# Performance work log

Hardware: AMD Instinct MI355X
Metric: run time of the kernel (lower is better)

Reference implementation:

```python
import jax, jax.numpy as jnp
import numpy as np

TOKENS, IN_F, OUT_F = 8192, 4096, 16384


def setup_inputs() -> dict:
    key = jax.random.key(0)
    k1, k2, k3, k4 = jax.random.split(key, 4)
    input = jax.random.normal(k1, (TOKENS, IN_F), dtype=jnp.float32)
    # int8 quantized weight, stored [out_features, in_features] like the torch buffer
    weight = jax.random.randint(k2, (OUT_F, IN_F), -127, 128, dtype=jnp.int8)
    # per-output-channel dequant scale
    weight_scale = jax.random.uniform(k3, (OUT_F,), dtype=jnp.float32, minval=0.001, maxval=0.02)
    bias = jax.random.normal(k4, (OUT_F,), dtype=jnp.float32) * 0.01
    return {"input": input, "weight": weight, "weight_scale": weight_scale, "bias": bias}


def reference(input, weight, weight_scale, bias):
    # Fallback path of DynamicQuantizeMatMul: dequantize B = weight.T * scale, then matmul.
    # B: [in_features, out_features]; scale broadcasts over out_features (columns).
    B = weight.astype(jnp.float32).T * weight_scale
    out = input @ B + bias  # [tokens, out_features]
    return out
```

## Files before the change

kernel.cpp:

```cpp
#include <hip/hip_runtime.h>

#define MDIM 8192
#define NDIM 16384
#define KDIM 4096

typedef int i32x4 __attribute__((ext_vector_type(4)));
typedef int i32x16 __attribute__((ext_vector_type(16)));
typedef float f32x4 __attribute__((ext_vector_type(4)));

__device__ __forceinline__ unsigned short f2bf(float f) {
  __bf16 h = (__bf16)f;
  return __builtin_bit_cast(unsigned short, h);
}

__device__ __forceinline__ void gload_lds16(const void* g, void* l) {
  __builtin_amdgcn_global_load_lds(
      (const __attribute__((address_space(1))) unsigned int*)g,
      (__attribute__((address_space(3))) unsigned int*)l, 16, 0, 0);
}


__global__ __launch_bounds__(256) void cvt_a_q8(const float* __restrict__ a,
                                                signed char* __restrict__ o,
                                                float* __restrict__ sA) {
  const int row = blockIdx.x;
  const int tid = threadIdx.x;
  float v[16];
  const float4* s4 = (const float4*)(a + (long long)row * KDIM + tid * 16);
#pragma unroll
  for (int i = 0; i < 4; ++i) {
    float4 f = s4[i];
    v[i * 4 + 0] = f.x; v[i * 4 + 1] = f.y;
    v[i * 4 + 2] = f.z; v[i * 4 + 3] = f.w;
  }
  float m = 0.f;
#pragma unroll
  for (int i = 0; i < 16; ++i) m = fmaxf(m, fabsf(v[i]));
#pragma unroll
  for (int off = 32; off; off >>= 1) m = fmaxf(m, __shfl_xor(m, off));
  __shared__ float red[4];
  if ((tid & 63) == 0) red[tid >> 6] = m;
  __syncthreads();
  m = fmaxf(fmaxf(red[0], red[1]), fmaxf(red[2], red[3]));
  const float inv = m > 0.f ? 127.f / m : 0.f;
  if (tid == 0) sA[row] = m * (1.f / 127.f);
  union { signed char c[16]; uint4 u; } p;
#pragma unroll
  for (int i = 0; i < 16; ++i)
    p.c[i] = (signed char)__float2int_rn(v[i] * inv);
  const int kt = tid >> 2, ks = tid & 3;
  *(uint4*)(o + ((((long long)(row >> 8) * 64 + kt) * 4 + ks) << 12) +
            ((row & 255) << 4)) = p.u;
}

__global__ __launch_bounds__(256) void cvt_w_q8(const int* __restrict__ w,
                                                signed char* __restrict__ o) {
  const int nt = blockIdx.x >> 6;
  const int kt = blockIdx.x & 63;
  const int t = threadIdx.x;
  const int* src = w + (long long)(nt * 256 + t) * KDIM + kt * 64;
  signed char* dst = o + (((long long)(nt * 64 + kt) * 4) << 12) + (t << 4);
#pragma unroll
  for (int ks = 0; ks < 4; ++ks) {
    union { signed char c[16]; uint4 u; } p;
#pragma unroll
    for (int i = 0; i < 4; ++i) {
      int4 x = *(const int4*)(src + ks * 16 + i * 4);
      p.c[i * 4 + 0] = (signed char)x.x; p.c[i * 4 + 1] = (signed char)x.y;
      p.c[i * 4 + 2] = (signed char)x.z; p.c[i * 4 + 3] = (signed char)x.w;
    }
    *(uint4*)(dst + (ks << 12)) = p.u;
  }
}

__global__ __launch_bounds__(512, 2) void gemm_i8_v13(
    const signed char* __restrict__ Ab, const signed char* __restrict__ Wb,
    const float* __restrict__ sA, const float* __restrict__ sc,
    const float* __restrict__ bi, float* __restrict__ out) {
  __shared__ alignas(16) char sm[3 * 32768];
  const int tid = threadIdx.x;
  const int lane = tid & 63;
  const int wv = tid >> 6;
  const int l31 = lane & 31;
  const int l32 = lane >> 5;
  const int wr = wv >> 2;
  const int wc = wv & 3;
  const int c = blockIdx.x & 7;
  const int l = blockIdx.x >> 3;
  const int mA = ((c & 3) << 3) + (l & 7);
  const int nT = ((c >> 2) << 5) + (l >> 3);
  const int bm = mA << 8;
  const int bn = nT << 8;

  int aO[2][4], bO[2][2];
#pragma unroll
  for (int kk = 0; kk < 2; ++kk) {
#pragma unroll
    for (int mb = 0; mb < 4; ++mb)
      aO[kk][mb] = (kk * 2 + l32) * 4096 + (wr * 128 + mb * 32 + l31) * 16;
#pragma unroll
    for (int nb = 0; nb < 2; ++nb)
      bO[kk][nb] = 16384 + (kk * 2 + l32) * 4096 + (wc * 64 + nb * 32 + l31) * 16;
  }

  i32x16 acc[4][2] = {};

  const signed char* aSrc = Ab + ((long long)mA << 20) + (tid << 4);
  const signed char* bSrc = Wb + ((long long)nT << 20) + (tid << 4);
  const int t16 = tid << 4;

  char* bR = &sm[0];
  char* bN = &sm[32768];
  char* bS = &sm[65536];

  auto STAGE = [&](char* slot) {
    gload_lds16(aSrc, slot + t16);
    gload_lds16(aSrc + 8192, slot + 8192 + t16);
    gload_lds16(bSrc, slot + 16384 + t16);
    gload_lds16(bSrc + 8192, slot + 24576 + t16);
    aSrc += 16384;
    bSrc += 16384;
  };

  STAGE(bR);
  STAGE(bN);
  asm volatile("s_waitcnt vmcnt(4)" ::: "memory");
  __builtin_amdgcn_s_barrier();

  for (int t = 0; t < 64; ++t) {
    if (t <= 61) STAGE(bS);
    __builtin_amdgcn_s_setprio(1);
    i32x4 aF[2][4], bF[2][2];
#pragma unroll
    for (int kk = 0; kk < 2; ++kk) {
#pragma unroll
      for (int mb = 0; mb < 4; ++mb) aF[kk][mb] = *(const i32x4*)(bR + aO[kk][mb]);
#pragma unroll
      for (int nb = 0; nb < 2; ++nb) bF[kk][nb] = *(const i32x4*)(bR + bO[kk][nb]);
    }
#pragma unroll
    for (int kk = 0; kk < 2; ++kk)
#pragma unroll
      for (int mb = 0; mb < 4; ++mb)
#pragma unroll
        for (int nb = 0; nb < 2; ++nb)
          acc[mb][nb] = __builtin_amdgcn_mfma_i32_32x32x32_i8(
              aF[kk][mb], bF[kk][nb], acc[mb][nb], 0, 0, 0);
    __builtin_amdgcn_s_setprio(0);
    if (t <= 61) {
      asm volatile("s_waitcnt vmcnt(4)" ::: "memory");
    } else if (t == 62) {
      asm volatile("s_waitcnt vmcnt(0)" ::: "memory");
    }
    if (t < 63) __builtin_amdgcn_s_barrier();
    char* tmp = bR; bR = bN; bN = bS; bS = tmp;
  }

  float sv[2], bv[2];
#pragma unroll
  for (int nb = 0; nb < 2; ++nb) {
    const int cc = bn + wc * 64 + nb * 32 + l31;
    sv[nb] = sc[cc];
    bv[nb] = bi[cc];
  }
#pragma unroll
  for (int mb = 0; mb < 4; ++mb) {
    const int rb = bm + wr * 128 + mb * 32 + l32 * 4;
    float sa[16];
#pragma unroll
    for (int r = 0; r < 16; ++r) sa[r] = sA[rb + (r & 3) + 8 * (r >> 2)];
#pragma unroll
    for (int nb = 0; nb < 2; ++nb) {
      const int cc = bn + wc * 64 + nb * 32 + l31;
#pragma unroll
      for (int r = 0; r < 16; ++r) {
        const long long row = rb + (r & 3) + 8 * (r >> 2);
        __builtin_nontemporal_store(
            (float)acc[mb][nb][r] * (sa[r] * sv[nb]) + bv[nb],
            out + row * NDIM + cc);
      }
    }
  }
}

__global__ __launch_bounds__(256, 2) void gemm_inline(
    const float* __restrict__ A, const int* __restrict__ W,
    const float* __restrict__ sc, const float* __restrict__ bi,
    float* __restrict__ out) {
  typedef __bf16 bf16x8 __attribute__((ext_vector_type(8)));
  __shared__ unsigned short As[128 * 72];
  __shared__ unsigned short Bs[128 * 72];
  const int tid = threadIdx.x;
  const int lane = tid & 63;
  const int wv = tid >> 6;
  const int wg = (blockIdx.x & 7) * 1024 + (blockIdx.x >> 3);
  const int bm = (wg & 63) * 128;
  const int bn = (wg >> 6) * 128;
  const int wr = (wv >> 1) * 64;
  const int wc = (wv & 1) * 64;
  const int r16 = lane & 15;
  const int g4 = lane >> 4;

  f32x4 acc[4][4] = {};

  const int srow = tid >> 4;
  const int sc4 = (tid & 15) << 2;
  const float* aPtr = A + (long long)(bm + srow) * KDIM + sc4;
  const int* wPtr = W + (long long)(bn + srow) * KDIM + sc4;

  for (int kt = 0; kt < KDIM; kt += 64) {
    float4 av[8];
    int4 wv4[8];
#pragma unroll
    for (int j = 0; j < 8; ++j)
      av[j] = *(const float4*)(aPtr + (long long)j * 16 * KDIM + kt);
#pragma unroll
    for (int j = 0; j < 8; ++j)
      wv4[j] = *(const int4*)(wPtr + (long long)j * 16 * KDIM + kt);
    __syncthreads();
#pragma unroll
    for (int j = 0; j < 8; ++j) {
      ushort4 u;
      u.x = f2bf(av[j].x); u.y = f2bf(av[j].y);
      u.z = f2bf(av[j].z); u.w = f2bf(av[j].w);
      *(ushort4*)&As[(srow + j * 16) * 72 + sc4] = u;
    }
#pragma unroll
    for (int j = 0; j < 8; ++j) {
      ushort4 u;
      u.x = f2bf((float)wv4[j].x); u.y = f2bf((float)wv4[j].y);
      u.z = f2bf((float)wv4[j].z); u.w = f2bf((float)wv4[j].w);
      *(ushort4*)&Bs[(srow + j * 16) * 72 + sc4] = u;
    }
    __syncthreads();
#pragma unroll
    for (int ks = 0; ks < 2; ++ks) {
      bf16x8 aF[4], bF[4];
      const int kofs = ks * 32 + g4 * 8;
#pragma unroll
      for (int m2 = 0; m2 < 4; ++m2)
        aF[m2] = *(const bf16x8*)&As[(wr + m2 * 16 + r16) * 72 + kofs];
#pragma unroll
      for (int n2 = 0; n2 < 4; ++n2)
        bF[n2] = *(const bf16x8*)&Bs[(wc + n2 * 16 + r16) * 72 + kofs];
#pragma unroll
      for (int m2 = 0; m2 < 4; ++m2)
#pragma unroll
        for (int n2 = 0; n2 < 4; ++n2)
          acc[m2][n2] = __builtin_amdgcn_mfma_f32_16x16x32_bf16(
              aF[m2], bF[n2], acc[m2][n2], 0, 0, 0);
    }
  }

  float sv[4], bv[4];
#pragma unroll
  for (int n2 = 0; n2 < 4; ++n2) {
    const int c = bn + wc + n2 * 16 + r16;
    sv[n2] = sc[c];
    bv[n2] = bi[c];
  }
#pragma unroll
  for (int m2 = 0; m2 < 4; ++m2) {
    const int row0 = bm + wr + m2 * 16 + g4 * 4;
#pragma unroll
    for (int n2 = 0; n2 < 4; ++n2) {
      const int c = bn + wc + n2 * 16 + r16;
      float* op = out + (long long)row0 * NDIM + c;
#pragma unroll
      for (int r = 0; r < 4; ++r)
        op[(long long)r * NDIM] = acc[m2][n2][r] * sv[n2] + bv[n2];
    }
  }
}

extern "C" void kernel_launch(void* const* d_in, const int* in_sizes, int n_in,
                              void* d_out, int out_size, void* d_ws, size_t ws_size,
                              hipStream_t stream) {
  const float* A = (const float*)d_in[0];
  const int* W = (const int*)d_in[1];
  const float* sc = (const float*)d_in[2];
  const float* bi = (const float*)d_in[3];
  float* out = (float*)d_out;

  const size_t needA = (size_t)MDIM * KDIM;
  const size_t needW = (size_t)NDIM * KDIM;
  const size_t offS = needA + needW;
  const size_t need = offS + (size_t)MDIM * 4;

  if (d_ws != nullptr && ws_size >= need) {
    signed char* Ab = (signed char*)d_ws;
    signed char* Wb = (signed char*)d_ws + needA;
    float* sA = (float*)((char*)d_ws + offS);
    cvt_a_q8<<<8192, 256, 0, stream>>>(A, Ab, sA);
    cvt_w_q8<<<4096, 256, 0, stream>>>(W, Wb);
    gemm_i8_v13<<<2048, 512, 0, stream>>>(Ab, Wb, sA, sc, bi, out);
  } else {
    gemm_inline<<<8192, 256, 0, stream>>>(A, W, sc, bi, out);
  }
}
```

Measured before the change: 656.7 us.

## Split each K-step into two half-phases with interleaved staging and barriers

The main loop now runs two phases per K-tile. Each phase issues half of the next tile's global-to-LDS loads (A in the first, B in the second), reads one kk slice of fragments from LDS, hits a barrier, then runs its 8 MFMAs. The aim is to interleave memory issue, LDS reads and matrix math more finely, in a ping-pong style across waves, and to halve fragment register pressure. The cost is two to three extra workgroup barriers per iteration, which can stall waves.

```diff
diff --git a/kernel.cpp b/kernel.cpp
--- a/kernel.cpp
+++ b/kernel.cpp
@@ -73,7 +73,7 @@
   }
 }
 
-__global__ __launch_bounds__(512, 2) void gemm_i8_v13(
+__global__ __launch_bounds__(512, 2) void gemm_i8_v18(
     const signed char* __restrict__ Ab, const signed char* __restrict__ Wb,
     const float* __restrict__ sA, const float* __restrict__ sc,
     const float* __restrict__ bi, float* __restrict__ out) {
@@ -113,39 +113,53 @@
   char* bN = &sm[32768];
   char* bS = &sm[65536];
 
-  auto STAGE = [&](char* slot) {
+  auto STAGE_P1 = [&](char* slot) {
     gload_lds16(aSrc, slot + t16);
     gload_lds16(aSrc + 8192, slot + 8192 + t16);
+  };
+  auto STAGE_P2 = [&](char* slot) {
     gload_lds16(bSrc, slot + 16384 + t16);
     gload_lds16(bSrc + 8192, slot + 24576 + t16);
     aSrc += 16384;
     bSrc += 16384;
   };
 
-  STAGE(bR);
-  STAGE(bN);
+  STAGE_P1(bR); STAGE_P2(bR);
+  STAGE_P1(bN); STAGE_P2(bN);
   asm volatile("s_waitcnt vmcnt(4)" ::: "memory");
   __builtin_amdgcn_s_barrier();
 
   for (int t = 0; t < 64; ++t) {
-    if (t <= 61) STAGE(bS);
+    if (t <= 61) STAGE_P1(bS);
+    i32x4 aF[4], bF[2];
+#pragma unroll
+    for (int mb = 0; mb < 4; ++mb) aF[mb] = *(const i32x4*)(bR + aO[0][mb]);
+#pragma unroll
+    for (int nb = 0; nb < 2; ++nb) bF[nb] = *(const i32x4*)(bR + bO[0][nb]);
+    __builtin_amdgcn_s_barrier();
     __builtin_amdgcn_s_setprio(1);
-    i32x4 aF[2][4], bF[2][2];
-#pragma unroll
-    for (int kk = 0; kk < 2; ++kk) {
-#pragma unroll
-      for (int mb = 0; mb < 4; ++mb) aF[kk][mb] = *(const i32x4*)(bR + aO[kk][mb]);
-#pragma unroll
-      for (int nb = 0; nb < 2; ++nb) bF[kk][nb] = *(const i32x4*)(bR + bO[kk][nb]);
-    }
-#pragma unroll
-    for (int kk = 0; kk < 2; ++kk)
-#pragma unroll
-      for (int mb = 0; mb < 4; ++mb)
-#pragma unroll
-        for (int nb = 0; nb < 2; ++nb)
-          acc[mb][nb] = __builtin_amdgcn_mfma_i32_32x32x32_i8(
-              aF[kk][mb], bF[kk][nb], acc[mb][nb], 0, 0, 0);
+#pragma unroll
+    for (int mb = 0; mb < 4; ++mb)
+#pragma unroll
+      for (int nb = 0; nb < 2; ++nb)
+        acc[mb][nb] = __builtin_amdgcn_mfma_i32_32x32x32_i8(
+            aF[mb], bF[nb], acc[mb][nb], 0, 0, 0);
+    __builtin_amdgcn_s_setprio(0);
+    __builtin_amdgcn_s_barrier();
+
+    if (t <= 61) STAGE_P2(bS);
+#pragma unroll
+    for (int mb = 0; mb < 4; ++mb) aF[mb] = *(const i32x4*)(bR + aO[1][mb]);
+#pragma unroll
+    for (int nb = 0; nb < 2; ++nb) bF[nb] = *(const i32x4*)(bR + bO[1][nb]);
+    __builtin_amdgcn_s_barrier();
+    __builtin_amdgcn_s_setprio(1);
+#pragma unroll
+    for (int mb = 0; mb < 4; ++mb)
+#pragma unroll
+      for (int nb = 0; nb < 2; ++nb)
+        acc[mb][nb] = __builtin_amdgcn_mfma_i32_32x32x32_i8(
+            aF[mb], bF[nb], acc[mb][nb], 0, 0, 0);
     __builtin_amdgcn_s_setprio(0);
     if (t <= 61) {
       asm volatile("s_waitcnt vmcnt(4)" ::: "memory");
@@ -293,7 +307,7 @@
     float* sA = (float*)((char*)d_ws + offS);
     cvt_a_q8<<<8192, 256, 0, stream>>>(A, Ab, sA);
     cvt_w_q8<<<4096, 256, 0, stream>>>(W, Wb);
-    gemm_i8_v13<<<2048, 512, 0, stream>>>(Ab, Wb, sA, sc, bi, out);
+    gemm_i8_v18<<<2048, 512, 0, stream>>>(Ab, Wb, sA, sc, bi, out);
   } else {
     gemm_inline<<<8192, 256, 0, stream>>>(A, W, sc, bi, out);
   }
```

Measured after the change: 645.0 us. No clear change (-1.8%).
